# Performance work log

Measured on AMD Instinct MI355X. Metric: run time of the kernel, lower is better.

Reference implementation:

```python
import jax, jax.numpy as jnp
import numpy as np

N = 100_000   # nodes
E = 3_200_000 # edges
G = 128       # graphs in batch
H = 32        # hidden_dim
PI = float(np.pi)


def setup_inputs() -> dict:
    key = jax.random.key(0)
    ks = jax.random.split(key, 18)
    p = lambda k, s: (jax.random.normal(k, s, dtype=jnp.float32) * 0.1)
    x = jax.random.normal(ks[0], (N, 1), dtype=jnp.float32)
    edge_index = jax.random.randint(ks[1], (2, E), 0, N, dtype=jnp.int32)
    batch = jnp.sort(jax.random.randint(ks[2], (N,), 0, G, dtype=jnp.int32))
    return dict(
        x=x, edge_index=edge_index, batch=batch,
        W1=p(ks[3], (1, H)),  b1=jnp.zeros((H,), jnp.float32),
        W2=p(ks[4], (H, H)),  b2=jnp.zeros((H,), jnp.float32),
        W3=p(ks[5], (H, H)),  b3=jnp.zeros((H,), jnp.float32),
        Wt1=p(ks[6], (H, 32)), bt1=jnp.zeros((32,), jnp.float32),
        Wt2=p(ks[7], (32, 1)), bt2=jnp.zeros((1,), jnp.float32),
        Wg1=p(ks[8], (H, 32)), bg1=jnp.zeros((32,), jnp.float32),
        Wg2=p(ks[9], (32, 2)), bg2=jnp.zeros((2,), jnp.float32),
    )


def _gcn_norm(edge_index):
    # PyG GCNConv default: add self-loops, symmetric normalization.
    loop = jnp.arange(N, dtype=edge_index.dtype)
    src = jnp.concatenate([edge_index[0], loop])
    dst = jnp.concatenate([edge_index[1], loop])
    deg = jax.ops.segment_sum(jnp.ones_like(dst, dtype=jnp.float32), dst, num_segments=N)
    dinv = jnp.where(deg > 0, jax.lax.rsqrt(jnp.maximum(deg, 1.0)), 0.0)
    norm = dinv[src] * dinv[dst]  # [E+N]
    return src, dst, norm


def _gcn_conv(x, W, b, src, dst, norm):
    h = x @ W                                  # [N, out]
    msg = h[src] * norm[:, None]               # gather + scale  [E+N, out]
    return jax.ops.segment_sum(msg, dst, num_segments=N) + b


def _forward(x, W1, b1, W2, b2, W3, b3, Wt1, bt1, Wt2, bt2, Wg1, bg1, Wg2, bg2,
             edge_index, batch):
    src, dst, norm = _gcn_norm(edge_index)
    x = jax.nn.relu(_gcn_conv(x, W1, b1, src, dst, norm))
    x = jax.nn.relu(_gcn_conv(x, W2, b2, src, dst, norm))
    h = jax.nn.relu(_gcn_conv(x, W3, b3, src, dst, norm))
    # theta head per node
    theta = PI * jax.nn.sigmoid(jax.nn.relu(h @ Wt1 + bt1) @ Wt2 + bt2)[:, 0]  # [N]
    # global mean pool per graph
    counts = jax.ops.segment_sum(jnp.ones((N,), jnp.float32), batch, num_segments=G)
    gsum = jax.ops.segment_sum(h, batch, num_segments=G)
    gemb = gsum / jnp.maximum(counts, 1.0)[:, None]                            # [G, H]
    beta_gamma = 2.0 * PI * jax.nn.sigmoid(jax.nn.relu(gemb @ Wg1 + bg1) @ Wg2 + bg2)  # [G, 2]
    return theta, beta_gamma


def reference(x, edge_index, batch, W1, b1, W2, b2, W3, b3,
              Wt1, bt1, Wt2, bt2, Wg1, bg1, Wg2, bg2):
    return _forward(x, W1, b1, W2, b2, W3, b3, Wt1, bt1, Wt2, bt2,
                    Wg1, bg1, Wg2, bg2, edge_index, batch)
```

## Files before the change

kernel.cpp:

```cpp
#include <hip/hip_runtime.h>
#include <hip/hip_bf16.h>

#define PI_F 3.14159265358979323846f
#define NBLK 256
#define BSH 8
#define BSZ 256
#define SCAP 10240

static inline size_t align256(size_t x) { return (x + 255) & ~size_t(255); }

__device__ __forceinline__ float bflo(unsigned w) { return __uint_as_float(w << 16); }
__device__ __forceinline__ float bfhi(unsigned w) { return __uint_as_float(w & 0xFFFF0000u); }
__device__ __forceinline__ unsigned bfpack(float a, float b) {
    unsigned lo = (__float_as_uint(a) + 0x8000u) >> 16;
    unsigned hi = (__float_as_uint(b) + 0x8000u) & 0xFFFF0000u;
    return lo | hi;
}

#define BF_ACC8Q(q) \
    acc[0] += bflo((q).x); acc[1] += bfhi((q).x); \
    acc[2] += bflo((q).y); acc[3] += bfhi((q).y); \
    acc[4] += bflo((q).z); acc[5] += bfhi((q).z); \
    acc[6] += bflo((q).w); acc[7] += bfhi((q).w);


__global__ void __launch_bounds__(1024) count_kernel(
                             const int* __restrict__ dst, int* __restrict__ C,
                             int E, int CHUNK, int NB2) {
    extern __shared__ int hist[];
    for (int i = threadIdx.x; i < NB2; i += 1024) hist[i] = 0;
    __syncthreads();
    int s0 = blockIdx.x * CHUNK, s1 = min(s0 + CHUNK, E);
    for (int e = s0 + threadIdx.x; e < s1; e += 1024)
        atomicAdd(&hist[dst[e] >> BSH], 1);
    __syncthreads();
    for (int i = threadIdx.x; i < NB2; i += 1024)
        C[(size_t)blockIdx.x * NB2 + i] = hist[i];
}

__global__ void scan_blocks_kernel(int* __restrict__ C, int* __restrict__ colsum, int NB2) {
    __shared__ int s[256];
    int k = blockIdx.x;
    int b = threadIdx.x;
    int v = C[(size_t)b * NB2 + k];
    s[b] = v;
    __syncthreads();
    for (int off = 1; off < 256; off <<= 1) {
        int w = (b >= off) ? s[b - off] : 0;
        __syncthreads();
        s[b] += w;
        __syncthreads();
    }
    C[(size_t)b * NB2 + k] = s[b] - v;
    if (b == 255) colsum[k] = s[255];
}

__global__ void scan_totals_kernel(const int* __restrict__ colsum, int* __restrict__ bbase,
                                   int NB2, int E) {
    __shared__ int s[256];
    __shared__ int running;
    if (threadIdx.x == 0) running = 0;
    __syncthreads();
    for (int base = 0; base < NB2; base += 256) {
        int i = base + threadIdx.x;
        int v = (i < NB2) ? colsum[i] : 0;
        s[threadIdx.x] = v;
        __syncthreads();
        for (int off = 1; off < 256; off <<= 1) {
            int w = (threadIdx.x >= (unsigned)off) ? s[threadIdx.x - off] : 0;
            __syncthreads();
            s[threadIdx.x] += w;
            __syncthreads();
        }
        if (i < NB2) bbase[i] = running + s[threadIdx.x] - v;
        __syncthreads();
        if (threadIdx.x == 255) running += s[255];
        __syncthreads();
    }
    if (threadIdx.x == 0) bbase[NB2] = E;
}

__global__ void __launch_bounds__(1024) scatter_kernel(
                               const int* __restrict__ src, const int* __restrict__ dst,
                               const int* __restrict__ C, const int* __restrict__ bbase,
                               unsigned* __restrict__ bkt_data, int E, int CHUNK, int NB2) {
    extern __shared__ int ofs[];
    for (int i = threadIdx.x; i < NB2; i += 1024)
        ofs[i] = bbase[i] + C[(size_t)blockIdx.x * NB2 + i];
    __syncthreads();
    int s0 = blockIdx.x * CHUNK, s1 = min(s0 + CHUNK, E);
    for (int e = s0 + threadIdx.x; e < s1; e += 1024) {
        int d = dst[e];
        int p = atomicAdd(&ofs[d >> BSH], 1);
        bkt_data[p] = ((unsigned)(d & (BSZ - 1)) << 17) | (unsigned)src[e];
    }
}

__global__ void __launch_bounds__(512) csr_build_kernel(
                                 const unsigned* __restrict__ bkt_data, const int* __restrict__ bbase,
                                 const float* __restrict__ x,
                                 unsigned* __restrict__ csr, int* __restrict__ e_start,
                                 float* __restrict__ dinv, float* __restrict__ xd,
                                 int N, int NB2) {
    __shared__ unsigned sdata[SCAP];
    __shared__ int hist[256];
    __shared__ int scn[256];
    __shared__ int bump[256];
    int tid = threadIdx.x;
    int b = blockIdx.x;
    int g0 = bbase[b], g1 = bbase[b + 1];
    int cnt = g1 - g0;
    bool fits = (cnt <= SCAP);
    if (tid < 256) hist[tid] = 0;
    __syncthreads();
    for (int i = tid; i < cnt; i += 512) {
        unsigned pk = bkt_data[g0 + i];
        if (fits) sdata[i] = pk;
        atomicAdd(&hist[pk >> 17], 1);
    }
    __syncthreads();
    int orig = (tid < 256) ? hist[tid] : 0;
    if (tid < 256) scn[tid] = orig;
    __syncthreads();
    for (int off = 1; off < 256; off <<= 1) {
        int w = (tid >= off && tid < 256) ? scn[tid - off] : 0;
        __syncthreads();
        if (tid < 256) scn[tid] += w;
        __syncthreads();
    }
    if (tid < 256) {
        int excl = scn[tid] - orig;
        bump[tid] = g0 + excl;
        int node = b * BSZ + tid;
        if (node < N) {
            float dv = rsqrtf((float)(orig + 1));
            dinv[node] = dv;
            xd[node] = x[node] * dv;
            e_start[node] = g0 + excl;
        }
    }
    if (b == NB2 - 1 && tid == 0) e_start[N] = g1;
    __syncthreads();
    for (int i = tid; i < cnt; i += 512) {
        unsigned pk = fits ? sdata[i] : bkt_data[g0 + i];
        int p = atomicAdd(&bump[pk >> 17], 1);
        csr[p] = pk & 0x1FFFFu;
    }
}


__device__ __forceinline__ void mm32_8(const float* __restrict__ sW, const float vr[8],
                                       int sub, int lane, float o[8]) {
    const float4* sW4 = (const float4*)sW;
    int base = lane & ~3;
#pragma unroll
    for (int r = 0; r < 4; r++) {
#pragma unroll
        for (int i = 0; i < 8; i++) {
            float vk = __shfl(vr[i], base | r, 64);
            int k = r * 8 + i;
            float4 w0 = sW4[k * 8 + sub * 2];
            float4 w1 = sW4[k * 8 + sub * 2 + 1];
            o[0] += vk * w0.x; o[1] += vk * w0.y; o[2] += vk * w0.z; o[3] += vk * w0.w;
            o[4] += vk * w1.x; o[5] += vk * w1.y; o[6] += vk * w1.z; o[7] += vk * w1.w;
        }
    }
}

__global__ void __launch_bounds__(256) agg1_kernel(
                            const float* __restrict__ xd, const int* __restrict__ e_start,
                            const unsigned* __restrict__ csr, const float* __restrict__ dinv,
                            const float* __restrict__ W1, const float* __restrict__ b1,
                            const float* __restrict__ W2,
                            unsigned short* __restrict__ ub, int n) {
    __shared__ float sW2[1024];
    __shared__ float sW1[32], sb1[32];
    for (int i = threadIdx.x; i < 1024; i += 256) sW2[i] = W2[i];
    if (threadIdx.x < 32) { sW1[threadIdx.x] = W1[threadIdx.x]; sb1[threadIdx.x] = b1[threadIdx.x]; }
    __syncthreads();
    int t = blockIdx.x * 256 + threadIdx.x;
    int d = t >> 2, sub = t & 3;
    int lane = threadIdx.x & 63;
    if (d >= n) return;
    int e0 = e_start[d];
    int cnt = e_start[d + 1] - e0;
    float s = 0.f;
    int j = sub;
    for (; j + 8 <= cnt; j += 8) {
        int i0 = (int)csr[e0 + j], i1 = (int)csr[e0 + j + 4];
        s += xd[i0]; s += xd[i1];
    }
    for (; j < cnt; j += 4) s += xd[(int)csr[e0 + j]];
    s += __shfl_xor(s, 1, 64);
    s += __shfl_xor(s, 2, 64);
    float dv = dinv[d];
    float tt = dv * (s + xd[d]);
    float vr[8];
#pragma unroll
    for (int i = 0; i < 8; i++) vr[i] = fmaxf(tt * sW1[sub * 8 + i] + sb1[sub * 8 + i], 0.f);
    float o[8];
#pragma unroll
    for (int i = 0; i < 8; i++) o[i] = 0.f;
    mm32_8(sW2, vr, sub, lane, o);
    unsigned ow[4];
#pragma unroll
    for (int i2 = 0; i2 < 4; i2++) ow[i2] = bfpack(dv * o[2 * i2], dv * o[2 * i2 + 1]);
    ((uint4*)ub)[(size_t)d * 4 + sub] = *(uint4*)&ow[0];
}

__global__ void __launch_bounds__(256) agg2_kernel(
                            const unsigned short* __restrict__ ub,
                            const int* __restrict__ e_start, const unsigned* __restrict__ csr,
                            const float* __restrict__ dinv, const float* __restrict__ bias,
                            const float* __restrict__ W,
                            unsigned short* __restrict__ ob, int n) {
    __shared__ float sW[1024];
    __shared__ float sb[32];
    for (int i = threadIdx.x; i < 1024; i += 256) sW[i] = W[i];
    if (threadIdx.x < 32) sb[threadIdx.x] = bias[threadIdx.x];
    __syncthreads();
    int t = blockIdx.x * 256 + threadIdx.x;
    int d = t >> 2, sub = t & 3;
    int lane = threadIdx.x & 63;
    if (d >= n) return;
    int e0 = e_start[d];
    int cnt = e_start[d + 1] - e0;
    float acc[8];
#pragma unroll
    for (int i = 0; i < 8; i++) acc[i] = 0.f;
    const uint4* rows = (const uint4*)ub;
    int j = 0;
    for (; j + 4 <= cnt; j += 4) {
        int i0 = (int)csr[e0 + j],     i1 = (int)csr[e0 + j + 1];
        int i2 = (int)csr[e0 + j + 2], i3 = (int)csr[e0 + j + 3];
        uint4 q0 = rows[(size_t)i0 * 4 + sub];
        uint4 q1 = rows[(size_t)i1 * 4 + sub];
        uint4 q2 = rows[(size_t)i2 * 4 + sub];
        uint4 q3 = rows[(size_t)i3 * 4 + sub];
        BF_ACC8Q(q0); BF_ACC8Q(q1); BF_ACC8Q(q2); BF_ACC8Q(q3);
    }
    for (; j < cnt; j++) {
        int i0 = (int)csr[e0 + j];
        uint4 q0 = rows[(size_t)i0 * 4 + sub];
        BF_ACC8Q(q0);
    }
    {
        uint4 q0 = rows[(size_t)d * 4 + sub];
        BF_ACC8Q(q0);
    }
    float dv = dinv[d];
    float vr[8];
#pragma unroll
    for (int i = 0; i < 8; i++) vr[i] = fmaxf(dv * acc[i] + sb[sub * 8 + i], 0.f);
    float o[8];
#pragma unroll
    for (int i = 0; i < 8; i++) o[i] = 0.f;
    mm32_8(sW, vr, sub, lane, o);
    unsigned ow[4];
#pragma unroll
    for (int i2 = 0; i2 < 4; i2++) ow[i2] = bfpack(dv * o[2 * i2], dv * o[2 * i2 + 1]);
    ((uint4*)ob)[(size_t)d * 4 + sub] = *(uint4*)&ow[0];
}

__global__ void __launch_bounds__(256) agg3_kernel(
                            const unsigned short* __restrict__ ub,
                            const int* __restrict__ e_start, const unsigned* __restrict__ csr,
                            const float* __restrict__ dinv, const float* __restrict__ bias,
                            const float* __restrict__ Wt1, const float* __restrict__ bt1,
                            const float* __restrict__ Wt2, const float* __restrict__ bt2,
                            unsigned short* __restrict__ hb, float* __restrict__ theta, int n) {
    __shared__ float sW[1024];
    __shared__ float sb[32], sbt[32], sw2[32];
    for (int i = threadIdx.x; i < 1024; i += 256) sW[i] = Wt1[i];
    if (threadIdx.x < 32) {
        sb[threadIdx.x] = bias[threadIdx.x];
        sbt[threadIdx.x] = bt1[threadIdx.x];
        sw2[threadIdx.x] = Wt2[threadIdx.x];
    }
    __syncthreads();
    int t = blockIdx.x * 256 + threadIdx.x;
    int d = t >> 2, sub = t & 3;
    int lane = threadIdx.x & 63;
    if (d >= n) return;
    int e0 = e_start[d];
    int cnt = e_start[d + 1] - e0;
    float acc[8];
#pragma unroll
    for (int i = 0; i < 8; i++) acc[i] = 0.f;
    const uint4* rows = (const uint4*)ub;
    int j = 0;
    for (; j + 4 <= cnt; j += 4) {
        int i0 = (int)csr[e0 + j],     i1 = (int)csr[e0 + j + 1];
        int i2 = (int)csr[e0 + j + 2], i3 = (int)csr[e0 + j + 3];
        uint4 q0 = rows[(size_t)i0 * 4 + sub];
        uint4 q1 = rows[(size_t)i1 * 4 + sub];
        uint4 q2 = rows[(size_t)i2 * 4 + sub];
        uint4 q3 = rows[(size_t)i3 * 4 + sub];
        BF_ACC8Q(q0); BF_ACC8Q(q1); BF_ACC8Q(q2); BF_ACC8Q(q3);
    }
    for (; j < cnt; j++) {
        int i0 = (int)csr[e0 + j];
        uint4 q0 = rows[(size_t)i0 * 4 + sub];
        BF_ACC8Q(q0);
    }
    {
        uint4 q0 = rows[(size_t)d * 4 + sub];
        BF_ACC8Q(q0);
    }
    float dv = dinv[d];
    float vr[8];
#pragma unroll
    for (int i = 0; i < 8; i++) vr[i] = fmaxf(dv * acc[i] + sb[sub * 8 + i], 0.f);
    unsigned ow[4];
#pragma unroll
    for (int i2 = 0; i2 < 4; i2++) ow[i2] = bfpack(vr[2 * i2], vr[2 * i2 + 1]);
    ((uint4*)hb)[(size_t)d * 4 + sub] = *(uint4*)&ow[0];
    float o[8];
#pragma unroll
    for (int i = 0; i < 8; i++) o[i] = 0.f;
    mm32_8(sW, vr, sub, lane, o);
    float tl = 0.f;
#pragma unroll
    for (int i = 0; i < 8; i++)
        tl += fmaxf(o[i] + sbt[sub * 8 + i], 0.f) * sw2[sub * 8 + i];
    tl += __shfl_xor(tl, 1, 64);
    tl += __shfl_xor(tl, 2, 64);
    if (sub == 0) theta[d] = PI_F / (1.f + __expf(-(tl + bt2[0])));
}


__global__ void gb_kernel(const int* __restrict__ batch, int* __restrict__ gstart,
                          int n, int G) {
    int i = blockIdx.x * 256 + threadIdx.x;
    if (i >= n) return;
    int g = batch[i];
    if (i == 0) {
        for (int gg = 0; gg <= g; gg++) gstart[gg] = 0;
    } else {
        int gp = batch[i - 1];
        for (int gg = gp + 1; gg <= g; gg++) gstart[gg] = i;
    }
    if (i == n - 1) {
        for (int gg = g + 1; gg <= G; gg++) gstart[gg] = n;
    }
}

__global__ void __launch_bounds__(512) bg_kernel(
                          const unsigned short* __restrict__ hb, const int* __restrict__ gstart,
                          const float* __restrict__ Wg1, const float* __restrict__ bg1v,
                          const float* __restrict__ Wg2, const float* __restrict__ bg2v,
                          float* __restrict__ out, int G) {
    __shared__ float sW[1024];
    __shared__ float part[8][32];
    for (int i = threadIdx.x; i < 1024; i += 512) sW[i] = Wg1[i];
    int g = blockIdx.x;
    int s = gstart[g], e = gstart[g + 1];
    int w = threadIdx.x >> 6;
    int lane = threadIdx.x & 63;
    int f = lane & 31, h = lane >> 5;
    float a = 0.f;
    for (int i = s + (w << 1) + h; i < e; i += 16)
        a += __uint_as_float((unsigned)hb[((size_t)i << 5) + f] << 16);
    a += __shfl_xor(a, 32, 64);
    if (h == 0) part[w][f] = a;
    __syncthreads();
    if (w == 0) {
        float hv = 0.f;
#pragma unroll
        for (int p = 0; p < 8; p++) hv += part[p][f];
        hv /= fmaxf((float)(e - s), 1.f);
        int base = lane & 32;
        float acc = bg1v[f];
#pragma unroll
        for (int k = 0; k < 32; k++) acc += __shfl(hv, base | k, 64) * sW[k * 32 + f];
        acc = fmaxf(acc, 0.f);
        float p0 = acc * Wg2[f * 2 + 0];
        float p1 = acc * Wg2[f * 2 + 1];
#pragma unroll
        for (int m = 1; m < 32; m <<= 1) {
            p0 += __shfl_xor(p0, m, 64);
            p1 += __shfl_xor(p1, m, 64);
        }
        if (lane == 0) {
            out[g * 2 + 0] = 2.f * PI_F / (1.f + __expf(-(p0 + bg2v[0])));
            out[g * 2 + 1] = 2.f * PI_F / (1.f + __expf(-(p1 + bg2v[1])));
        }
    }
}


extern "C" void kernel_launch(void* const* d_in, const int* in_sizes, int n_in,
                              void* d_out, int out_size, void* d_ws, size_t ws_size,
                              hipStream_t stream) {
    const float* x   = (const float*)d_in[0];
    const int*   ei  = (const int*)d_in[1];
    const int* batch = (const int*)d_in[2];
    const float* W1  = (const float*)d_in[3];
    const float* b1  = (const float*)d_in[4];
    const float* W2  = (const float*)d_in[5];
    const float* b2  = (const float*)d_in[6];
    const float* W3  = (const float*)d_in[7];
    const float* b3  = (const float*)d_in[8];
    const float* Wt1 = (const float*)d_in[9];
    const float* bt1 = (const float*)d_in[10];
    const float* Wt2 = (const float*)d_in[11];
    const float* bt2 = (const float*)d_in[12];
    const float* Wg1 = (const float*)d_in[13];
    const float* bg1 = (const float*)d_in[14];
    const float* Wg2 = (const float*)d_in[15];
    const float* bg2 = (const float*)d_in[16];

    const int N = in_sizes[0];
    const int E = in_sizes[1] / 2;
    const int G = 128;
    const int* src = ei;
    const int* dst = ei + E;
    float* theta_out = (float*)d_out;
    float* bg_out = (float*)d_out + N;

    const int NB2 = (N + BSZ - 1) >> BSH;
    const int CHUNK = (E + NBLK - 1) / NBLK;

    char* w = (char*)d_ws;
    auto alloc = [&](size_t bytes) -> char* { char* p = w; w += align256(bytes); return p; };
    int*      C        = (int*)alloc((size_t)NBLK * NB2 * 4);
    int*      colsum   = (int*)alloc((size_t)NB2 * 4);
    int*      bbase    = (int*)alloc((size_t)(NB2 + 1) * 4);
    unsigned* bkt_data = (unsigned*)alloc((size_t)E * 4);
    unsigned* csr      = (unsigned*)alloc((size_t)E * 4);
    int*      e_start  = (int*)alloc((size_t)(N + 1) * 4);
    float*    dinv     = (float*)alloc((size_t)N * 4);
    float*    xd       = (float*)alloc((size_t)N * 4);
    unsigned short* u2b = (unsigned short*)alloc((size_t)N * 64);
    unsigned short* u3b = (unsigned short*)alloc((size_t)N * 64);
    unsigned short* hb  = (unsigned short*)alloc((size_t)N * 64);
    int*      gstart   = (int*)alloc((size_t)(G + 1) * 4);

    size_t ldsB = (size_t)NB2 * 4;
    count_kernel<<<NBLK, 1024, ldsB, stream>>>(dst, C, E, CHUNK, NB2);
    scan_blocks_kernel<<<NB2, 256, 0, stream>>>(C, colsum, NB2);
    scan_totals_kernel<<<1, 256, 0, stream>>>(colsum, bbase, NB2, E);
    scatter_kernel<<<NBLK, 1024, ldsB, stream>>>(src, dst, C, bbase, bkt_data, E, CHUNK, NB2);
    csr_build_kernel<<<NB2, 512, 0, stream>>>(bkt_data, bbase, x, csr, e_start, dinv, xd, N, NB2);
    gb_kernel<<<(N + 255) / 256, 256, 0, stream>>>(batch, gstart, N, G);

    unsigned gridQ = (unsigned)(((size_t)N * 4 + 255) / 256);

    agg1_kernel<<<gridQ, 256, 0, stream>>>(xd, e_start, csr, dinv, W1, b1, W2, u2b, N);
    agg2_kernel<<<gridQ, 256, 0, stream>>>(u2b, e_start, csr, dinv, b2, W3, u3b, N);
    agg3_kernel<<<gridQ, 256, 0, stream>>>(u3b, e_start, csr, dinv, b3,
                                           Wt1, bt1, Wt2, bt2, hb, theta_out, N);

    bg_kernel<<<G, 512, 0, stream>>>(hb, gstart, Wg1, bg1, Wg2, bg2, bg_out, G);
}
```

Measured before the change: 294.6 us.

## Store intermediate node features as per-row scaled FP8 instead of BF16

Intermediate feature rows between GCN layers are now quantized to FP8 with a per-node absmax scale instead of BF16. This halves the bytes per gathered row in the edge aggregation kernels, at the cost of one extra scale load per edge. Unpacking uses the hardware packed FP8 convert instructions. It risks accuracy loss from the much lower mantissa precision.

```diff
diff --git a/kernel.cpp b/kernel.cpp
--- a/kernel.cpp
+++ b/kernel.cpp
@@ -9,19 +9,22 @@
 
 static inline size_t align256(size_t x) { return (x + 255) & ~size_t(255); }
 
-__device__ __forceinline__ float bflo(unsigned w) { return __uint_as_float(w << 16); }
-__device__ __forceinline__ float bfhi(unsigned w) { return __uint_as_float(w & 0xFFFF0000u); }
+typedef float v2f __attribute__((ext_vector_type(2)));
+
 __device__ __forceinline__ unsigned bfpack(float a, float b) {
     unsigned lo = (__float_as_uint(a) + 0x8000u) >> 16;
     unsigned hi = (__float_as_uint(b) + 0x8000u) & 0xFFFF0000u;
     return lo | hi;
 }
 
-#define BF_ACC8Q(q) \
-    acc[0] += bflo((q).x); acc[1] += bfhi((q).x); \
-    acc[2] += bflo((q).y); acc[3] += bfhi((q).y); \
-    acc[4] += bflo((q).z); acc[5] += bfhi((q).z); \
-    acc[6] += bflo((q).w); acc[7] += bfhi((q).w);
+__device__ __forceinline__ void f8acc(uint2 q, float rs, float acc[8]) {
+    v2f l0 = __builtin_amdgcn_cvt_pk_f32_fp8(q.x, false);
+    v2f h0 = __builtin_amdgcn_cvt_pk_f32_fp8(q.x, true);
+    v2f l1 = __builtin_amdgcn_cvt_pk_f32_fp8(q.y, false);
+    v2f h1 = __builtin_amdgcn_cvt_pk_f32_fp8(q.y, true);
+    acc[0] += rs * l0.x; acc[1] += rs * l0.y; acc[2] += rs * h0.x; acc[3] += rs * h0.y;
+    acc[4] += rs * l1.x; acc[5] += rs * l1.y; acc[6] += rs * h1.x; acc[7] += rs * h1.y;
+}
 
 
 __global__ void __launch_bounds__(1024) count_kernel(
@@ -167,12 +170,31 @@
     }
 }
 
+__device__ __forceinline__ void store_f8(unsigned char* __restrict__ u8, float* __restrict__ uscale,
+                                         int d, int sub, const float o[8]) {
+    float am = 0.f;
+#pragma unroll
+    for (int i = 0; i < 8; i++) am = fmaxf(am, fabsf(o[i]));
+    am = fmaxf(am, __shfl_xor(am, 1, 64));
+    am = fmaxf(am, __shfl_xor(am, 2, 64));
+    float rm = fmaxf(am, 1e-20f);
+    float sc = 128.f / rm;
+    unsigned w0 = 0, w1 = 0;
+    w0 = __builtin_amdgcn_cvt_pk_fp8_f32(o[0] * sc, o[1] * sc, w0, false);
+    w0 = __builtin_amdgcn_cvt_pk_fp8_f32(o[2] * sc, o[3] * sc, w0, true);
+    w1 = __builtin_amdgcn_cvt_pk_fp8_f32(o[4] * sc, o[5] * sc, w1, false);
+    w1 = __builtin_amdgcn_cvt_pk_fp8_f32(o[6] * sc, o[7] * sc, w1, true);
+    uint2 st; st.x = w0; st.y = w1;
+    ((uint2*)u8)[(size_t)d * 4 + sub] = st;
+    if (sub == 0) uscale[d] = rm * (1.f / 128.f);
+}
+
 __global__ void __launch_bounds__(256) agg1_kernel(
                             const float* __restrict__ xd, const int* __restrict__ e_start,
                             const unsigned* __restrict__ csr, const float* __restrict__ dinv,
                             const float* __restrict__ W1, const float* __restrict__ b1,
                             const float* __restrict__ W2,
-                            unsigned short* __restrict__ ub, int n) {
+                            unsigned char* __restrict__ u8o, float* __restrict__ uso, int n) {
     __shared__ float sW2[1024];
     __shared__ float sW1[32], sb1[32];
     for (int i = threadIdx.x; i < 1024; i += 256) sW2[i] = W2[i];
@@ -202,18 +224,46 @@
 #pragma unroll
     for (int i = 0; i < 8; i++) o[i] = 0.f;
     mm32_8(sW2, vr, sub, lane, o);
-    unsigned ow[4];
-#pragma unroll
-    for (int i2 = 0; i2 < 4; i2++) ow[i2] = bfpack(dv * o[2 * i2], dv * o[2 * i2 + 1]);
-    ((uint4*)ub)[(size_t)d * 4 + sub] = *(uint4*)&ow[0];
+#pragma unroll
+    for (int i = 0; i < 8; i++) o[i] *= dv;
+    store_f8(u8o, uso, d, sub, o);
+}
+
+__device__ __forceinline__ void gather_f8(const unsigned char* __restrict__ u8,
+                                          const float* __restrict__ uscale,
+                                          const unsigned* __restrict__ csr,
+                                          int e0, int cnt, int d, int sub, float acc[8]) {
+#pragma unroll
+    for (int i = 0; i < 8; i++) acc[i] = 0.f;
+    const uint2* rows = (const uint2*)u8;
+    int j = 0;
+    for (; j + 4 <= cnt; j += 4) {
+        int i0 = (int)csr[e0 + j],     i1 = (int)csr[e0 + j + 1];
+        int i2 = (int)csr[e0 + j + 2], i3 = (int)csr[e0 + j + 3];
+        float r0 = uscale[i0], r1 = uscale[i1], r2 = uscale[i2], r3 = uscale[i3];
+        uint2 q0 = rows[(size_t)i0 * 4 + sub];
+        uint2 q1 = rows[(size_t)i1 * 4 + sub];
+        uint2 q2 = rows[(size_t)i2 * 4 + sub];
+        uint2 q3 = rows[(size_t)i3 * 4 + sub];
+        f8acc(q0, r0, acc); f8acc(q1, r1, acc); f8acc(q2, r2, acc); f8acc(q3, r3, acc);
+    }
+    for (; j < cnt; j++) {
+        int i0 = (int)csr[e0 + j];
+        float r0 = uscale[i0];
+        uint2 q0 = rows[(size_t)i0 * 4 + sub];
+        f8acc(q0, r0, acc);
+    }
+    float rs = uscale[d];
+    uint2 qs = rows[(size_t)d * 4 + sub];
+    f8acc(qs, rs, acc);
 }
 
 __global__ void __launch_bounds__(256) agg2_kernel(
-                            const unsigned short* __restrict__ ub,
+                            const unsigned char* __restrict__ u8, const float* __restrict__ uscale,
                             const int* __restrict__ e_start, const unsigned* __restrict__ csr,
                             const float* __restrict__ dinv, const float* __restrict__ bias,
                             const float* __restrict__ W,
-                            unsigned short* __restrict__ ob, int n) {
+                            unsigned char* __restrict__ o8, float* __restrict__ oscale, int n) {
     __shared__ float sW[1024];
     __shared__ float sb[32];
     for (int i = threadIdx.x; i < 1024; i += 256) sW[i] = W[i];
@@ -226,28 +276,7 @@
     int e0 = e_start[d];
     int cnt = e_start[d + 1] - e0;
     float acc[8];
-#pragma unroll
-    for (int i = 0; i < 8; i++) acc[i] = 0.f;
-    const uint4* rows = (const uint4*)ub;
-    int j = 0;
-    for (; j + 4 <= cnt; j += 4) {
-        int i0 = (int)csr[e0 + j],     i1 = (int)csr[e0 + j + 1];
-        int i2 = (int)csr[e0 + j + 2], i3 = (int)csr[e0 + j + 3];
-        uint4 q0 = rows[(size_t)i0 * 4 + sub];
-        uint4 q1 = rows[(size_t)i1 * 4 + sub];
-        uint4 q2 = rows[(size_t)i2 * 4 + sub];
-        uint4 q3 = rows[(size_t)i3 * 4 + sub];
-        BF_ACC8Q(q0); BF_ACC8Q(q1); BF_ACC8Q(q2); BF_ACC8Q(q3);
-    }
-    for (; j < cnt; j++) {
-        int i0 = (int)csr[e0 + j];
-        uint4 q0 = rows[(size_t)i0 * 4 + sub];
-        BF_ACC8Q(q0);
-    }
-    {
-        uint4 q0 = rows[(size_t)d * 4 + sub];
-        BF_ACC8Q(q0);
-    }
+    gather_f8(u8, uscale, csr, e0, cnt, d, sub, acc);
     float dv = dinv[d];
     float vr[8];
 #pragma unroll
@@ -256,14 +285,13 @@
 #pragma unroll
     for (int i = 0; i < 8; i++) o[i] = 0.f;
     mm32_8(sW, vr, sub, lane, o);
-    unsigned ow[4];
-#pragma unroll
-    for (int i2 = 0; i2 < 4; i2++) ow[i2] = bfpack(dv * o[2 * i2], dv * o[2 * i2 + 1]);
-    ((uint4*)ob)[(size_t)d * 4 + sub] = *(uint4*)&ow[0];
+#pragma unroll
+    for (int i = 0; i < 8; i++) o[i] *= dv;
+    store_f8(o8, oscale, d, sub, o);
 }
 
 __global__ void __launch_bounds__(256) agg3_kernel(
-                            const unsigned short* __restrict__ ub,
+                            const unsigned char* __restrict__ u8, const float* __restrict__ uscale,
                             const int* __restrict__ e_start, const unsigned* __restrict__ csr,
                             const float* __restrict__ dinv, const float* __restrict__ bias,
                             const float* __restrict__ Wt1, const float* __restrict__ bt1,
@@ -285,28 +313,7 @@
     int e0 = e_start[d];
     int cnt = e_start[d + 1] - e0;
     float acc[8];
-#pragma unroll
-    for (int i = 0; i < 8; i++) acc[i] = 0.f;
-    const uint4* rows = (const uint4*)ub;
-    int j = 0;
-    for (; j + 4 <= cnt; j += 4) {
-        int i0 = (int)csr[e0 + j],     i1 = (int)csr[e0 + j + 1];
-        int i2 = (int)csr[e0 + j + 2], i3 = (int)csr[e0 + j + 3];
-        uint4 q0 = rows[(size_t)i0 * 4 + sub];
-        uint4 q1 = rows[(size_t)i1 * 4 + sub];
-        uint4 q2 = rows[(size_t)i2 * 4 + sub];
-        uint4 q3 = rows[(size_t)i3 * 4 + sub];
-        BF_ACC8Q(q0); BF_ACC8Q(q1); BF_ACC8Q(q2); BF_ACC8Q(q3);
-    }
-    for (; j < cnt; j++) {
-        int i0 = (int)csr[e0 + j];
-        uint4 q0 = rows[(size_t)i0 * 4 + sub];
-        BF_ACC8Q(q0);
-    }
-    {
-        uint4 q0 = rows[(size_t)d * 4 + sub];
-        BF_ACC8Q(q0);
-    }
+    gather_f8(u8, uscale, csr, e0, cnt, d, sub, acc);
     float dv = dinv[d];
     float vr[8];
 #pragma unroll
@@ -431,9 +438,11 @@
     int*      e_start  = (int*)alloc((size_t)(N + 1) * 4);
     float*    dinv     = (float*)alloc((size_t)N * 4);
     float*    xd       = (float*)alloc((size_t)N * 4);
-    unsigned short* u2b = (unsigned short*)alloc((size_t)N * 64);
-    unsigned short* u3b = (unsigned short*)alloc((size_t)N * 64);
-    unsigned short* hb  = (unsigned short*)alloc((size_t)N * 64);
+    unsigned char* u2  = (unsigned char*)alloc((size_t)N * 32);
+    float*    us2      = (float*)alloc((size_t)N * 4);
+    unsigned char* u3  = (unsigned char*)alloc((size_t)N * 32);
+    float*    us3      = (float*)alloc((size_t)N * 4);
+    unsigned short* hb = (unsigned short*)alloc((size_t)N * 64);
     int*      gstart   = (int*)alloc((size_t)(G + 1) * 4);
 
     size_t ldsB = (size_t)NB2 * 4;
@@ -446,9 +455,9 @@
 
     unsigned gridQ = (unsigned)(((size_t)N * 4 + 255) / 256);
 
-    agg1_kernel<<<gridQ, 256, 0, stream>>>(xd, e_start, csr, dinv, W1, b1, W2, u2b, N);
-    agg2_kernel<<<gridQ, 256, 0, stream>>>(u2b, e_start, csr, dinv, b2, W3, u3b, N);
-    agg3_kernel<<<gridQ, 256, 0, stream>>>(u3b, e_start, csr, dinv, b3,
+    agg1_kernel<<<gridQ, 256, 0, stream>>>(xd, e_start, csr, dinv, W1, b1, W2, u2, us2, N);
+    agg2_kernel<<<gridQ, 256, 0, stream>>>(u2, us2, e_start, csr, dinv, b2, W3, u3, us3, N);
+    agg3_kernel<<<gridQ, 256, 0, stream>>>(u3, us3, e_start, csr, dinv, b3,
                                            Wt1, bt1, Wt2, bt2, hb, theta_out, N);
 
     bg_kernel<<<G, 512, 0, stream>>>(hb, gstart, Wg1, bg1, Wg2, bg2, bg_out, G);
```

Measured after the change: 287.8 us. 2.3% less time.
